# Optimization experiments

Measured on AMD Instinct MI355X. Metric: run time of the kernel, lower is better.

## Reference

```python
import jax, jax.numpy as jnp
import numpy as np

B, S, D = 4, 2048, 2048


def setup_inputs() -> dict:
    key = jax.random.key(0)
    ks = jax.random.split(key, 24)
    sc = 1.0 / np.sqrt(D)
    def lin(ki, kb):
        W = jax.random.normal(ks[ki], (D, D), dtype=jnp.float32) * sc
        b = jax.random.normal(ks[kb], (D,), dtype=jnp.float32) * 0.01
        return W, b
    Wi, bWi = lin(0, 1); Ui, bUi = lin(2, 3)
    Wf, bWf = lin(4, 5); Uf, bUf = lin(6, 7)
    Wc, bWc = lin(8, 9); Uc, bUc = lin(10, 11)
    Wo, bWo = lin(12, 13); Uo, bUo = lin(14, 15)
    Wp, bp = lin(16, 17)
    x = jax.random.normal(ks[18], (B, S, D), dtype=jnp.float32)
    h = jax.random.normal(ks[19], (B, S, D), dtype=jnp.float32)
    return dict(x=x, h=h, Wi=Wi, bWi=bWi, Ui=Ui, bUi=bUi,
                Wf=Wf, bWf=bWf, Uf=Uf, bUf=bUf,
                Wc=Wc, bWc=bWc, Uc=Uc, bUc=bUc,
                Wo=Wo, bWo=bWo, Uo=Uo, bUo=bUo,
                Wp=Wp, bp=bp)


def reference(x, h, Wi, bWi, Ui, bUi, Wf, bWf, Uf, bUf,
              Wc, bWc, Uc, bUc, Wo, bWo, Uo, bUo, Wp, bp):
    # In the torch source, h[:, t, :] is read BEFORE being overwritten at step t,
    # and c is zero-initialized with each slot written once (so f * c_prev == 0).
    # Hence the computation is exactly parallel over the time axis.
    Zi = jnp.einsum('bsd,ed->bse', x, Wi) + bWi + jnp.einsum('bsd,ed->bse', h, Ui) + bUi
    Zf = jnp.einsum('bsd,ed->bse', x, Wf) + bWf + jnp.einsum('bsd,ed->bse', h, Uf) + bUf
    Zc = jnp.einsum('bsd,ed->bse', x, Wc) + bWc + jnp.einsum('bsd,ed->bse', h, Uc) + bUc
    Zo = jnp.einsum('bsd,ed->bse', x, Wo) + bWo + jnp.einsum('bsd,ed->bse', h, Uo) + bUo
    i = jnp.exp(Zi)
    f = jnp.exp(Zf)  # multiplies a zero cell state in the source; kept for fidelity
    c = f * jnp.zeros_like(f) + i * jnp.tanh(Zc)
    h_out = jax.nn.sigmoid(Zo) * jnp.tanh(c)
    hidden_state = h_out[:, -1, :] @ Wp.T + bp
    return (hidden_state, c)
```

## Files before the change

kernel.cpp:

```cpp
#include <hip/hip_runtime.h>
#include <hip/hip_bf16.h>

typedef short short8 __attribute__((ext_vector_type(8)));
typedef unsigned short ushort8v __attribute__((ext_vector_type(8)));
typedef float f32x4 __attribute__((ext_vector_type(4)));

#define D_DIM 2048
#define KTOT 4096
#define M_TOT 8192


__device__ __forceinline__ unsigned short f2bf(float f) {
    union { float f; unsigned u; } c; c.f = f;
    unsigned u = c.u;
    u += 0x7fffu + ((u >> 16) & 1u);
    return (unsigned short)(u >> 16);
}

__device__ __forceinline__ float fast_tanh(float x) {
    float ax = fabsf(x);
    float ez = __expf(2.0f * fminf(ax, 15.0f));
    float t = (ez - 1.0f) / (ez + 1.0f);
    return copysignf(t, x);
}

#define GLOAD_LDS16(g, l)                                                     \
    __builtin_amdgcn_global_load_lds(                                         \
        (const __attribute__((address_space(1))) void*)(g),                   \
        (__attribute__((address_space(3))) void*)(l), 16, 0, 0)


__global__ __launch_bounds__(256)
void pack2(const float* __restrict__ X, const float* __restrict__ H,
           __hip_bfloat16* __restrict__ dst, int total8) {
    int t = blockIdx.x * 256 + threadIdx.x;
    if (t >= total8) return;
    long e0 = (long)t * 8;
    long r  = e0 >> 12;
    int  k  = (int)(e0 & 4095);
    const float* src = (k < D_DIM) ? (X + r * D_DIM + k)
                                   : (H + r * D_DIM + (k - D_DIM));
    float4 v0 = *(const float4*)(src);
    float4 v1 = *(const float4*)(src + 4);
    ushort8v o;
    o[0] = f2bf(v0.x); o[1] = f2bf(v0.y); o[2] = f2bf(v0.z); o[3] = f2bf(v0.w);
    o[4] = f2bf(v1.x); o[5] = f2bf(v1.y); o[6] = f2bf(v1.z); o[7] = f2bf(v1.w);
    *(ushort8v*)(dst + e0) = o;
}


#define BM 128
#define BN 128
#define BK 64

__global__ __launch_bounds__(256, 2)
void gemm_gates(const __hip_bfloat16* __restrict__ A,
                const __hip_bfloat16* __restrict__ Bi,
                const __hip_bfloat16* __restrict__ Bc,
                const float* __restrict__ bWi, const float* __restrict__ bUi,
                const float* __restrict__ bWc, const float* __restrict__ bUc,
                float* __restrict__ Cout) {
    __shared__ __hip_bfloat16 lds[3 * BM * BK];

    const int tid  = threadIdx.x;
    const int wid  = tid >> 6;
    const int lane = tid & 63;

    int bid = blockIdx.x;
    bid = (bid & 7) * 128 + (bid >> 3);
    const int tn = (bid & 15) * BN;
    const int tm = (bid >> 4) * BM;

    const int wr = (wid >> 1) * 64;
    const int wc = (wid & 1) * 64;

    f32x4 acc_i[4][4] = {};
    f32x4 acc_c[4][4] = {};

    const int crow = lane >> 3;
    const int ccol = (lane & 7) * 8;
    char* ldsB = (char*)lds;

    const int r15 = lane & 15;
    const int kh  = (lane >> 4) * 8;

    for (int k0 = 0; k0 < KTOT; k0 += BK) {
        __syncthreads();
        #pragma unroll
        for (int q = 0; q < 4; ++q) {
            const int ch  = wid * 4 + q;
            const int row = ch * 8 + crow;
            const __hip_bfloat16* gA = A  + (size_t)(tm + row) * KTOT + k0 + ccol;
            const __hip_bfloat16* gI = Bi + (size_t)(tn + row) * KTOT + k0 + ccol;
            const __hip_bfloat16* gC = Bc + (size_t)(tn + row) * KTOT + k0 + ccol;
            GLOAD_LDS16(gA, ldsB + ch * 1024);
            GLOAD_LDS16(gI, ldsB + 16384 + ch * 1024);
            GLOAD_LDS16(gC, ldsB + 32768 + ch * 1024);
        }
        __syncthreads();

        const __hip_bfloat16* lA = lds;
        const __hip_bfloat16* lI = lds + BM * BK;
        const __hip_bfloat16* lC = lds + 2 * BM * BK;

        #pragma unroll
        for (int kk = 0; kk < 2; ++kk) {
            const int kc = kk * 32 + kh;
            short8 af[4], fi[4], fc[4];
            #pragma unroll
            for (int m = 0; m < 4; ++m)
                af[m] = *(const short8*)(lA + (wr + m * 16 + r15) * BK + kc);
            #pragma unroll
            for (int n = 0; n < 4; ++n) {
                fi[n] = *(const short8*)(lI + (wc + n * 16 + r15) * BK + kc);
                fc[n] = *(const short8*)(lC + (wc + n * 16 + r15) * BK + kc);
            }
            #pragma unroll
            for (int m = 0; m < 4; ++m)
                #pragma unroll
                for (int n = 0; n < 4; ++n) {
                    acc_i[m][n] = __builtin_amdgcn_mfma_f32_16x16x32_bf16(
                        af[m], fi[n], acc_i[m][n], 0, 0, 0);
                    acc_c[m][n] = __builtin_amdgcn_mfma_f32_16x16x32_bf16(
                        af[m], fc[n], acc_c[m][n], 0, 0, 0);
                }
        }
    }

    const int rg = lane >> 4;
    #pragma unroll
    for (int n = 0; n < 4; ++n) {
        const int gn = tn + wc + n * 16 + r15;
        const float bi_ = bWi[gn] + bUi[gn];
        const float bc_ = bWc[gn] + bUc[gn];
        #pragma unroll
        for (int m = 0; m < 4; ++m) {
            #pragma unroll
            for (int r = 0; r < 4; ++r) {
                const int gm = tm + wr + m * 16 + rg * 4 + r;
                const float zi = acc_i[m][n][r] + bi_;
                const float zc = acc_c[m][n][r] + bc_;
                Cout[(size_t)gm * D_DIM + gn] = __expf(zi) * fast_tanh(zc);
            }
        }
    }
}


__global__ __launch_bounds__(256)
void last_gate(const float* __restrict__ x, const float* __restrict__ h,
               const float* __restrict__ Wo, const float* __restrict__ bWo,
               const float* __restrict__ Uo, const float* __restrict__ bUo,
               const float* __restrict__ cfull, float* __restrict__ hbuf) {
    const int o    = blockIdx.x * 4 + (threadIdx.x >> 6);
    const int lane = threadIdx.x & 63;
    const int b = o >> 11, e = o & 2047;
    const float* xr = x  + ((size_t)b * D_DIM + (D_DIM - 1)) * D_DIM;
    const float* hr = h  + ((size_t)b * D_DIM + (D_DIM - 1)) * D_DIM;
    const float* wo = Wo + (size_t)e * D_DIM;
    const float* uo = Uo + (size_t)e * D_DIM;
    float s = 0.0f;
    for (int d = lane; d < D_DIM; d += 64)
        s += xr[d] * wo[d] + hr[d] * uo[d];
    #pragma unroll
    for (int off = 32; off; off >>= 1) s += __shfl_down(s, off);
    if (lane == 0) {
        const float zo  = s + bWo[e] + bUo[e];
        const float sig = 1.0f / (1.0f + __expf(-zo));
        const float cv  = cfull[((size_t)b * D_DIM + (D_DIM - 1)) * D_DIM + e];
        hbuf[o] = sig * fast_tanh(cv);
    }
}


__global__ __launch_bounds__(256)
void proj(const float* __restrict__ hbuf, const float* __restrict__ Wp,
          const float* __restrict__ bp, float* __restrict__ out) {
    const int o    = blockIdx.x * 4 + (threadIdx.x >> 6);
    const int lane = threadIdx.x & 63;
    const int b = o >> 11, p = o & 2047;
    const float* hv = hbuf + (size_t)b * D_DIM;
    const float* wp = Wp   + (size_t)p * D_DIM;
    float s = 0.0f;
    for (int e = lane; e < D_DIM; e += 64)
        s += hv[e] * wp[e];
    #pragma unroll
    for (int off = 32; off; off >>= 1) s += __shfl_down(s, off);
    if (lane == 0) out[o] = s + bp[p];
}


extern "C" void kernel_launch(void* const* d_in, const int* in_sizes, int n_in,
                              void* d_out, int out_size, void* d_ws, size_t ws_size,
                              hipStream_t stream) {
    const float* x   = (const float*)d_in[0];
    const float* h   = (const float*)d_in[1];
    const float* Wi  = (const float*)d_in[2];  const float* bWi = (const float*)d_in[3];
    const float* Ui  = (const float*)d_in[4];  const float* bUi = (const float*)d_in[5];
    const float* Wc  = (const float*)d_in[10]; const float* bWc = (const float*)d_in[11];
    const float* Uc  = (const float*)d_in[12]; const float* bUc = (const float*)d_in[13];
    const float* Wo  = (const float*)d_in[14]; const float* bWo = (const float*)d_in[15];
    const float* Uo  = (const float*)d_in[16]; const float* bUo = (const float*)d_in[17];
    const float* Wp  = (const float*)d_in[18]; const float* bp  = (const float*)d_in[19];

    float* out = (float*)d_out;
    char*  ws  = (char*)d_ws;

    __hip_bfloat16* Abf  = (__hip_bfloat16*)ws;
    __hip_bfloat16* Bibf = (__hip_bfloat16*)(ws + ((size_t)64 << 20));
    __hip_bfloat16* Bcbf = (__hip_bfloat16*)(ws + ((size_t)80 << 20));
    float*          hbuf = (float*)(ws + ((size_t)96 << 20));

    pack2<<<16384, 256, 0, stream>>>(x,  h,  Abf,  M_TOT * KTOT / 8);
    pack2<<<4096,  256, 0, stream>>>(Wi, Ui, Bibf, D_DIM * KTOT / 8);
    pack2<<<4096,  256, 0, stream>>>(Wc, Uc, Bcbf, D_DIM * KTOT / 8);

    gemm_gates<<<(M_TOT / BM) * (D_DIM / BN), 256, 0, stream>>>(
        Abf, Bibf, Bcbf, bWi, bUi, bWc, bUc, out + 8192);

    last_gate<<<2048, 256, 0, stream>>>(x, h, Wo, bWo, Uo, bUo, out + 8192,
                                        (float*)hbuf);
    proj<<<2048, 256, 0, stream>>>(hbuf, Wp, bp, out);
}
```

Measured before the change: 376.1 us.

## Interleave gate weights into one matrix and use pipelined 256x256 GEMM

Packs Wi/Ui and Wc/Uc into a single interleaved B matrix (16-row groups alternating i and c gates) so one GEMM produces both gates per tile. The GEMM moves to 256x256 tiles with 8 waves, double-buffered LDS with XOR swizzle, staged prefetch interleaved with MFMA phases, and s_setprio around the compute. The aim is more reuse per loaded byte, hidden global-load latency and fewer LDS bank conflicts. The cost is more registers, a more complex barrier and waitcnt schedule, and a fused weight-pack kernel.

```diff
diff --git a/kernel.cpp b/kernel.cpp
--- a/kernel.cpp
+++ b/kernel.cpp
@@ -8,6 +8,7 @@
 #define D_DIM 2048
 #define KTOT 4096
 #define M_TOT 8192
+#define NPACK 4096
 
 
 __device__ __forceinline__ unsigned short f2bf(float f) {
@@ -49,98 +50,176 @@
 }
 
 
-#define BM 128
-#define BN 128
+__global__ __launch_bounds__(256)
+void pack_gates(const float* __restrict__ Wi, const float* __restrict__ Ui,
+                const float* __restrict__ Wc, const float* __restrict__ Uc,
+                __hip_bfloat16* __restrict__ dst) {
+    int t = blockIdx.x * 256 + threadIdx.x;
+    const int g = t >> 9;
+    const int k = (t & 511) * 8;
+    const int w = g & 31;
+    const int n = ((g >> 5) << 4) | (w & 15);
+    const float* Wm = (w & 16) ? Wc : Wi;
+    const float* Um = (w & 16) ? Uc : Ui;
+    const float* src = (k < D_DIM) ? (Wm + (size_t)n * D_DIM + k)
+                                   : (Um + (size_t)n * D_DIM + (k - D_DIM));
+    float4 v0 = *(const float4*)(src);
+    float4 v1 = *(const float4*)(src + 4);
+    ushort8v o;
+    o[0] = f2bf(v0.x); o[1] = f2bf(v0.y); o[2] = f2bf(v0.z); o[3] = f2bf(v0.w);
+    o[4] = f2bf(v1.x); o[5] = f2bf(v1.y); o[6] = f2bf(v1.z); o[7] = f2bf(v1.w);
+    *(ushort8v*)(dst + (size_t)g * KTOT + k) = o;
+}
+
+
 #define BK 64
-
-__global__ __launch_bounds__(256, 2)
-void gemm_gates(const __hip_bfloat16* __restrict__ A,
-                const __hip_bfloat16* __restrict__ Bi,
-                const __hip_bfloat16* __restrict__ Bc,
-                const float* __restrict__ bWi, const float* __restrict__ bUi,
-                const float* __restrict__ bWc, const float* __restrict__ bUc,
-                float* __restrict__ Cout) {
-    __shared__ __hip_bfloat16 lds[3 * BM * BK];
+#define NT (KTOT / BK)
+
+__device__ __forceinline__ void stage_half(const __hip_bfloat16* __restrict__ mat,
+                                           __hip_bfloat16* ldsHalf,
+                                           int rowbase, int kcol0,
+                                           int wid, int lane) {
+    #pragma unroll
+    for (int j = 0; j < 2; ++j) {
+        const int Lb  = wid * 128 + j * 64;
+        const int L   = Lb + lane;
+        const int row = L >> 2;
+        const int ul  = (L & 3) ^ (row & 3);
+        const __hip_bfloat16* src =
+            mat + (size_t)(rowbase + row) * KTOT + kcol0 + ul * 8;
+        GLOAD_LDS16(src, (char*)ldsHalf + Lb * 16);
+    }
+}
+
+__global__ __launch_bounds__(512, 2)
+void gemm8(const __hip_bfloat16* __restrict__ A,
+           const __hip_bfloat16* __restrict__ Bp,
+           const float* __restrict__ bWi, const float* __restrict__ bUi,
+           const float* __restrict__ bWc, const float* __restrict__ bUc,
+           float* __restrict__ Cout) {
+    __shared__ __hip_bfloat16 sA[2][2][256][32];
+    __shared__ __hip_bfloat16 sB[2][2][256][32];
 
     const int tid  = threadIdx.x;
     const int wid  = tid >> 6;
     const int lane = tid & 63;
 
     int bid = blockIdx.x;
-    bid = (bid & 7) * 128 + (bid >> 3);
-    const int tn = (bid & 15) * BN;
-    const int tm = (bid >> 4) * BM;
-
-    const int wr = (wid >> 1) * 64;
-    const int wc = (wid & 1) * 64;
-
-    f32x4 acc_i[4][4] = {};
-    f32x4 acc_c[4][4] = {};
-
-    const int crow = lane >> 3;
-    const int ccol = (lane & 7) * 8;
-    char* ldsB = (char*)lds;
-
+    bid = (bid & 7) * 64 + (bid >> 3);
+    const int tn = (bid & 15) * 256;
+    const int tm = (bid >> 4) * 256;
+
+    const int wr  = (wid >> 2) * 128;
+    const int wc  = (wid & 3) * 64;
     const int r15 = lane & 15;
-    const int kh  = (lane >> 4) * 8;
-
-    for (int k0 = 0; k0 < KTOT; k0 += BK) {
-        __syncthreads();
-        #pragma unroll
-        for (int q = 0; q < 4; ++q) {
-            const int ch  = wid * 4 + q;
-            const int row = ch * 8 + crow;
-            const __hip_bfloat16* gA = A  + (size_t)(tm + row) * KTOT + k0 + ccol;
-            const __hip_bfloat16* gI = Bi + (size_t)(tn + row) * KTOT + k0 + ccol;
-            const __hip_bfloat16* gC = Bc + (size_t)(tn + row) * KTOT + k0 + ccol;
-            GLOAD_LDS16(gA, ldsB + ch * 1024);
-            GLOAD_LDS16(gI, ldsB + 16384 + ch * 1024);
-            GLOAD_LDS16(gC, ldsB + 32768 + ch * 1024);
-        }
-        __syncthreads();
-
-        const __hip_bfloat16* lA = lds;
-        const __hip_bfloat16* lI = lds + BM * BK;
-        const __hip_bfloat16* lC = lds + 2 * BM * BK;
-
-        #pragma unroll
-        for (int kk = 0; kk < 2; ++kk) {
-            const int kc = kk * 32 + kh;
-            short8 af[4], fi[4], fc[4];
-            #pragma unroll
-            for (int m = 0; m < 4; ++m)
-                af[m] = *(const short8*)(lA + (wr + m * 16 + r15) * BK + kc);
-            #pragma unroll
-            for (int n = 0; n < 4; ++n) {
-                fi[n] = *(const short8*)(lI + (wc + n * 16 + r15) * BK + kc);
-                fc[n] = *(const short8*)(lC + (wc + n * 16 + r15) * BK + kc);
-            }
-            #pragma unroll
-            for (int m = 0; m < 4; ++m)
-                #pragma unroll
-                for (int n = 0; n < 4; ++n) {
-                    acc_i[m][n] = __builtin_amdgcn_mfma_f32_16x16x32_bf16(
-                        af[m], fi[n], acc_i[m][n], 0, 0, 0);
-                    acc_c[m][n] = __builtin_amdgcn_mfma_f32_16x16x32_bf16(
-                        af[m], fc[n], acc_c[m][n], 0, 0, 0);
-                }
-        }
+    const int uswz16 = ((lane >> 4) ^ (r15 & 3)) * 16;
+
+    f32x4 acc[8][4] = {};
+
+    stage_half(A,  &sA[0][0][0][0], tm, 0,  wid, lane);
+    stage_half(Bp, &sB[0][0][0][0], tn, 0,  wid, lane);
+    stage_half(A,  &sA[0][1][0][0], tm, 32, wid, lane);
+    stage_half(Bp, &sB[0][1][0][0], tn, 32, wid, lane);
+    asm volatile("s_waitcnt vmcnt(4)" ::: "memory");
+    __builtin_amdgcn_s_barrier();
+
+    short8 af[4], bf[4];
+
+    for (int t = 0; t < NT; ++t) {
+        const int cur = t & 1, nxt = cur ^ 1;
+        const bool pf = (t + 1 < NT);
+        const int kc1 = (t + 1) * BK;
+        const char* pA = (const char*)sA[cur];
+        const char* pB = (const char*)sB[cur];
+
+        #pragma unroll
+        for (int m = 0; m < 4; ++m)
+            af[m] = *(const short8*)(pA + (size_t)(wr + m * 16 + r15) * 64 + uswz16);
+        #pragma unroll
+        for (int n = 0; n < 4; ++n)
+            bf[n] = *(const short8*)(pB + (size_t)(wc + n * 16 + r15) * 64 + uswz16);
+        if (pf) stage_half(A, &sA[nxt][0][0][0], tm, kc1, wid, lane);
+        __builtin_amdgcn_s_barrier();
+        asm volatile("s_waitcnt lgkmcnt(0)" ::: "memory");
+        __builtin_amdgcn_s_setprio(1);
+        #pragma unroll
+        for (int m = 0; m < 4; ++m)
+            #pragma unroll
+            for (int n = 0; n < 4; ++n)
+                acc[m][n] = __builtin_amdgcn_mfma_f32_16x16x32_bf16(
+                    af[m], bf[n], acc[m][n], 0, 0, 0);
+        __builtin_amdgcn_s_setprio(0);
+        __builtin_amdgcn_s_barrier();
+
+        #pragma unroll
+        for (int m = 0; m < 4; ++m)
+            af[m] = *(const short8*)(pA + (size_t)(wr + 64 + m * 16 + r15) * 64 + uswz16);
+        if (pf) stage_half(Bp, &sB[nxt][0][0][0], tn, kc1, wid, lane);
+        __builtin_amdgcn_s_barrier();
+        asm volatile("s_waitcnt lgkmcnt(0)" ::: "memory");
+        __builtin_amdgcn_s_setprio(1);
+        #pragma unroll
+        for (int m = 0; m < 4; ++m)
+            #pragma unroll
+            for (int n = 0; n < 4; ++n)
+                acc[4 + m][n] = __builtin_amdgcn_mfma_f32_16x16x32_bf16(
+                    af[m], bf[n], acc[4 + m][n], 0, 0, 0);
+        __builtin_amdgcn_s_setprio(0);
+        if (t < NT - 1) asm volatile("s_waitcnt vmcnt(4)" ::: "memory");
+        else            asm volatile("s_waitcnt vmcnt(0)" ::: "memory");
+        __builtin_amdgcn_s_barrier();
+
+        #pragma unroll
+        for (int m = 0; m < 4; ++m)
+            af[m] = *(const short8*)(pA + 16384 + (size_t)(wr + m * 16 + r15) * 64 + uswz16);
+        #pragma unroll
+        for (int n = 0; n < 4; ++n)
+            bf[n] = *(const short8*)(pB + 16384 + (size_t)(wc + n * 16 + r15) * 64 + uswz16);
+        if (pf) stage_half(A, &sA[nxt][1][0][0], tm, kc1 + 32, wid, lane);
+        __builtin_amdgcn_s_barrier();
+        asm volatile("s_waitcnt lgkmcnt(0)" ::: "memory");
+        __builtin_amdgcn_s_setprio(1);
+        #pragma unroll
+        for (int m = 0; m < 4; ++m)
+            #pragma unroll
+            for (int n = 0; n < 4; ++n)
+                acc[m][n] = __builtin_amdgcn_mfma_f32_16x16x32_bf16(
+                    af[m], bf[n], acc[m][n], 0, 0, 0);
+        __builtin_amdgcn_s_setprio(0);
+        __builtin_amdgcn_s_barrier();
+
+        #pragma unroll
+        for (int m = 0; m < 4; ++m)
+            af[m] = *(const short8*)(pA + 16384 + (size_t)(wr + 64 + m * 16 + r15) * 64 + uswz16);
+        if (pf) stage_half(Bp, &sB[nxt][1][0][0], tn, kc1 + 32, wid, lane);
+        __builtin_amdgcn_s_barrier();
+        asm volatile("s_waitcnt lgkmcnt(0)" ::: "memory");
+        __builtin_amdgcn_s_setprio(1);
+        #pragma unroll
+        for (int m = 0; m < 4; ++m)
+            #pragma unroll
+            for (int n = 0; n < 4; ++n)
+                acc[4 + m][n] = __builtin_amdgcn_mfma_f32_16x16x32_bf16(
+                    af[m], bf[n], acc[4 + m][n], 0, 0, 0);
+        __builtin_amdgcn_s_setprio(0);
+        asm volatile("s_waitcnt vmcnt(4)" ::: "memory");
+        __builtin_amdgcn_s_barrier();
     }
 
-    const int rg = lane >> 4;
+    const int rg4 = (lane >> 4) * 4;
     #pragma unroll
-    for (int n = 0; n < 4; ++n) {
-        const int gn = tn + wc + n * 16 + r15;
+    for (int q = 0; q < 2; ++q) {
+        const int gn = (tn >> 1) + (wc >> 1) + q * 16 + r15;
         const float bi_ = bWi[gn] + bUi[gn];
         const float bc_ = bWc[gn] + bUc[gn];
         #pragma unroll
-        for (int m = 0; m < 4; ++m) {
+        for (int m = 0; m < 8; ++m) {
+            const int gm = tm + wr + m * 16 + rg4;
             #pragma unroll
             for (int r = 0; r < 4; ++r) {
-                const int gm = tm + wr + m * 16 + rg * 4 + r;
-                const float zi = acc_i[m][n][r] + bi_;
-                const float zc = acc_c[m][n][r] + bc_;
-                Cout[(size_t)gm * D_DIM + gn] = __expf(zi) * fast_tanh(zc);
+                const float zi = acc[m][2 * q][r]     + bi_;
+                const float zc = acc[m][2 * q + 1][r] + bc_;
+                Cout[(size_t)(gm + r) * D_DIM + gn] = __expf(zi) * fast_tanh(zc);
             }
         }
     }
@@ -207,16 +286,14 @@
     char*  ws  = (char*)d_ws;
 
     __hip_bfloat16* Abf  = (__hip_bfloat16*)ws;
-    __hip_bfloat16* Bibf = (__hip_bfloat16*)(ws + ((size_t)64 << 20));
-    __hip_bfloat16* Bcbf = (__hip_bfloat16*)(ws + ((size_t)80 << 20));
+    __hip_bfloat16* Bpk  = (__hip_bfloat16*)(ws + ((size_t)64 << 20));
     float*          hbuf = (float*)(ws + ((size_t)96 << 20));
 
-    pack2<<<16384, 256, 0, stream>>>(x,  h,  Abf,  M_TOT * KTOT / 8);
-    pack2<<<4096,  256, 0, stream>>>(Wi, Ui, Bibf, D_DIM * KTOT / 8);
-    pack2<<<4096,  256, 0, stream>>>(Wc, Uc, Bcbf, D_DIM * KTOT / 8);
-
-    gemm_gates<<<(M_TOT / BM) * (D_DIM / BN), 256, 0, stream>>>(
-        Abf, Bibf, Bcbf, bWi, bUi, bWc, bUc, out + 8192);
+    pack2<<<16384, 256, 0, stream>>>(x, h, Abf, M_TOT * KTOT / 8);
+    pack_gates<<<8192, 256, 0, stream>>>(Wi, Ui, Wc, Uc, Bpk);
+
+    gemm8<<<(M_TOT / 256) * (NPACK / 256), 512, 0, stream>>>(
+        Abf, Bpk, bWi, bUi, bWc, bUc, out + 8192);
 
     last_gate<<<2048, 256, 0, stream>>>(x, h, Wo, bWo, Uo, bUo, out + 8192,
                                         (float*)hbuf);
```

Result: slower. 406.4 us (+8.1%).
